# Kernel optimization log

Measured on AMD Instinct MI355X. Metric: run time of the kernel, lower is better.

## Reference

```python
import jax, jax.numpy as jnp
import numpy as np

SEQ_LEN = 2048
EMBED = 1024
HIDDEN = 1024
BATCH = 4


def setup_inputs() -> dict:
    key = jax.random.key(0)
    ks = jax.random.split(key, 7)
    # xavier_uniform for weights: limit = sqrt(6/(fan_in+fan_out))
    lim = float(np.sqrt(6.0 / (EMBED + HIDDEN)))
    blim = float(1.0 / np.sqrt(EMBED))  # torch Linear default bias init U(-1/sqrt(fan_in), ...)
    inputs = jax.random.normal(ks[0], (BATCH, SEQ_LEN, EMBED), dtype=jnp.float32)
    Wq = jax.random.uniform(ks[1], (HIDDEN, EMBED), jnp.float32, -lim, lim)
    Wk = jax.random.uniform(ks[2], (HIDDEN, EMBED), jnp.float32, -lim, lim)
    Wv = jax.random.uniform(ks[3], (HIDDEN, EMBED), jnp.float32, -lim, lim)
    bq = jax.random.uniform(ks[4], (HIDDEN,), jnp.float32, -blim, blim)
    bk = jax.random.uniform(ks[5], (HIDDEN,), jnp.float32, -blim, blim)
    bv = jax.random.uniform(ks[6], (HIDDEN,), jnp.float32, -blim, blim)
    return {"inputs": inputs, "Wq": Wq, "bq": bq, "Wk": Wk, "bk": bk, "Wv": Wv, "bv": bv}


def reference(inputs, Wq, bq, Wk, bk, Wv, bv):
    B, S, E = inputs.shape
    q = jnp.einsum('bse,he->bsh', inputs, Wq) + bq  # [B,S,H]
    k = jnp.einsum('bse,he->bsh', inputs, Wk) + bk
    v = jnp.einsum('bse,he->bsh', inputs, Wv) + bv
    # NOTE: source scales by 1/sqrt(embed_size), not hidden_size
    scores = jnp.einsum('bqh,bkh->bqk', q, k) / jnp.sqrt(jnp.float32(E))
    causal = jnp.tril(jnp.ones((S, S), dtype=bool))  # [S,S]
    scores = jnp.where(causal[None, :, :], scores, -jnp.inf)
    attn = jax.nn.softmax(scores, axis=-1)
    return jnp.einsum('bqk,bkh->bqh', attn, v)
```

## Files before the change

kernel.cpp:

```cpp
#include <hip/hip_runtime.h>
#include <cstdint>
#include <cstddef>
#include <math.h>

typedef unsigned short u16;

#define S_LEN 2048
#define EMB   1024
#define HID   1024
#define NB    4

using bf16x8 = __attribute__((ext_vector_type(8))) __bf16;
using f32x4  = __attribute__((ext_vector_type(4))) float;


__device__ __forceinline__ u16 f2bf(float f) {
  union { float f; uint32_t u; } c; c.f = f;
  uint32_t u = c.u;
  uint32_t r = (u + 0x7fffu + ((u >> 16) & 1u)) >> 16;
  return (u16)r;
}

__device__ __forceinline__ void gld_lds16(const u16* g, u16* l) {
  auto gp = (const __attribute__((address_space(1))) uint32_t*)(uintptr_t)(const void*)g;
  auto lp = (__attribute__((address_space(3))) uint32_t*)(uintptr_t)(void*)l;
  __builtin_amdgcn_global_load_lds(gp, lp, 16, 0, 0);
}


__global__ void cvt_f32_bf16(const float* __restrict__ in, u16* __restrict__ out, int n4) {
  int i = blockIdx.x * blockDim.x + threadIdx.x;
  int stride = gridDim.x * blockDim.x;
  for (; i < n4; i += stride) {
    float4 v = reinterpret_cast<const float4*>(in)[i];
    reinterpret_cast<ushort4*>(out)[i] =
      make_ushort4(f2bf(v.x), f2bf(v.y), f2bf(v.z), f2bf(v.w));
  }
}

__global__ void cvt3_f32_bf16(const float* __restrict__ a, const float* __restrict__ b,
                              const float* __restrict__ c, u16* __restrict__ out, int n4) {
  const float* src = (blockIdx.y == 0) ? a : (blockIdx.y == 1) ? b : c;
  u16* dst = out + (size_t)blockIdx.y * (size_t)n4 * 4;
  int i = blockIdx.x * blockDim.x + threadIdx.x;
  int stride = gridDim.x * blockDim.x;
  for (; i < n4; i += stride) {
    float4 v = reinterpret_cast<const float4*>(src)[i];
    reinterpret_cast<ushort4*>(dst)[i] =
      make_ushort4(f2bf(v.x), f2bf(v.y), f2bf(v.z), f2bf(v.w));
  }
}


template<int EPI>
__global__ __launch_bounds__(512, 2)
void gemmT(const u16* __restrict__ A, const u16* __restrict__ Bw, void* __restrict__ Cv,
           const float* __restrict__ b0, const float* __restrict__ b1,
           const float* __restrict__ b2, u16* __restrict__ VT,
           int N, long sA, long sB, long sC, float scale)
{
  constexpr int K = 1024;
  constexpr int NTILE = K / 64;
  const int z = blockIdx.z;
  A  += (long)z * sA;
  Bw += (long)z * sB;

  __shared__ __align__(16) u16 smem[32768];

  const int tid = threadIdx.x;
  const int l   = tid & 63;
  const int w   = tid >> 6;
  const int wr  = w >> 2;
  const int wc  = w & 3;

  int bm, bn;
  if constexpr (EPI == 2) {
    const int x0 = blockIdx.x;
    const int x  = (x0 & 7) * ((int)gridDim.x >> 3) + (x0 >> 3);
    int bi = (int)((sqrtf(8.0f * (float)x + 1.0f) - 1.0f) * 0.5f);
    while ((bi + 1) * (bi + 2) / 2 <= x) ++bi;
    while (bi * (bi + 1) / 2 > x) --bi;
    bm = bi * 128;
    bn = (x - bi * (bi + 1) / 2) * 128;
  } else {
    const int nwg = gridDim.x * gridDim.y;
    const int lin = blockIdx.y * gridDim.x + blockIdx.x;
    const int sw  = (lin & 7) * (nwg >> 3) + (lin >> 3);
    bm = (sw / gridDim.x) * 128;
    bn = (sw % gridDim.x) * 128;
  }

  const int arow = w * 16 + (l >> 2);
  const int acs  = (l & 3) ^ (((l >> 5) & 1) << 1);
  const u16* gbA = A  + (long)(bm + arow) * K + acs * 8;
  const u16* gbB = Bw + (long)(bn + arow) * K + acs * 8;

#define STGH(t, s, dbase)                                                       \
  do {                                                                          \
    const long _o = (long)(t) * 64 + (s) * 32;                                  \
    gld_lds16(gbA + _o, smem + (dbase) + (s) * 4096 + w * 512);                 \
    gld_lds16(gbB + _o, smem + (dbase) + 8192 + (s) * 4096 + w * 512);          \
  } while (0)

  const int lr  = l & 15;
  const int kg  = l >> 4;
  const int kgp = kg ^ (((lr >> 3) & 1) << 1);
  int aoff[4], boff[2];
#pragma unroll
  for (int m = 0; m < 4; ++m) aoff[m] = (wr * 64 + m * 16 + lr) * 32 + kgp * 8;
#pragma unroll
  for (int n = 0; n < 2; ++n) boff[n] = (wc * 32 + n * 16 + lr) * 32 + kgp * 8;

  f32x4 acc[4][2] = {};

  STGH(0, 0, 0);
  STGH(0, 1, 0);
  asm volatile("s_waitcnt vmcnt(0)" ::: "memory");
  __builtin_amdgcn_s_barrier();
  asm volatile("" ::: "memory");

#define PHASE(d, s, STGSTMT)                                                    \
  do {                                                                          \
    const u16* hA = smem + (d) * 16384 + (s) * 4096;                            \
    const u16* hB = smem + (d) * 16384 + 8192 + (s) * 4096;                     \
    bf16x8 av[4], bv[2];                                                        \
    _Pragma("unroll")                                                           \
    for (int m_ = 0; m_ < 4; ++m_)                                              \
      av[m_] = *reinterpret_cast<const bf16x8*>(hA + aoff[m_]);                 \
    _Pragma("unroll")                                                           \
    for (int n_ = 0; n_ < 2; ++n_)                                              \
      bv[n_] = *reinterpret_cast<const bf16x8*>(hB + boff[n_]);                 \
    STGSTMT;                                                                    \
    asm volatile("s_waitcnt vmcnt(2)" ::: "memory");                            \
    __builtin_amdgcn_s_barrier();                                               \
    asm volatile("" ::: "memory");                                              \
    __builtin_amdgcn_s_setprio(1);                                              \
    _Pragma("unroll")                                                           \
    for (int m_ = 0; m_ < 4; ++m_)                                              \
      _Pragma("unroll")                                                         \
      for (int n_ = 0; n_ < 2; ++n_)                                            \
        acc[m_][n_] = __builtin_amdgcn_mfma_f32_16x16x32_bf16(                  \
            av[m_], bv[n_], acc[m_][n_], 0, 0, 0);                              \
    __builtin_amdgcn_s_setprio(0);                                              \
    asm volatile("" ::: "memory");                                              \
  } while (0)

#pragma unroll 1
  for (int i = 0; i < NTILE / 2; ++i) {
    const int t1 = 2 * i + 1;
    const int t2 = (2 * i + 2 < NTILE) ? 2 * i + 2 : NTILE - 1;
    PHASE(0, 0, STGH(t1, 0, 16384));
    PHASE(0, 1, STGH(t1, 1, 16384));
    PHASE(1, 0, STGH(t2, 0, 0));
    PHASE(1, 1, STGH(t2, 1, 0));
  }
#undef PHASE
#undef STGH

  if constexpr (EPI == 2) {
    float* C = (float*)Cv + (long)z * sC;
#pragma unroll
    for (int n = 0; n < 2; ++n) {
      const int col = bn + wc * 32 + n * 16 + lr;
#pragma unroll
      for (int m = 0; m < 4; ++m) {
        const int row0 = bm + wr * 64 + m * 16 + kg * 4;
#pragma unroll
        for (int q = 0; q < 4; ++q) {
          const int row = row0 + q;
          float v = acc[m][n][q] * scale;
          if (col > row) v = -1e30f;
          C[(long)row * N + col] = v;
        }
      }
    }
  } else {
    constexpr long M = (long)NB * S_LEN;
    const int sel = bn >> 10;
    const float* bias = (sel == 0) ? b0 : (sel == 1) ? b1 : b2;
    u16* QK = (u16*)Cv;
#pragma unroll
    for (int n = 0; n < 2; ++n) {
      const int col = bn + wc * 32 + n * 16 + lr;
      const int h   = col & (HID - 1);
      const float bbv = bias[h];
#pragma unroll
      for (int m = 0; m < 4; ++m) {
        const int row0 = bm + wr * 64 + m * 16 + kg * 4;
        if (sel < 2) {
          u16* dst = QK + (long)sel * M * HID + (long)row0 * HID + h;
#pragma unroll
          for (int q = 0; q < 4; ++q)
            dst[(long)q * HID] = f2bf(acc[m][n][q] + bbv);
        } else {
          const int b = row0 >> 11;
          const int s = row0 & (S_LEN - 1);
          ushort4 o = make_ushort4(f2bf(acc[m][n][0] + bbv), f2bf(acc[m][n][1] + bbv),
                                   f2bf(acc[m][n][2] + bbv), f2bf(acc[m][n][3] + bbv));
          *reinterpret_cast<ushort4*>(VT + ((long)b * HID + h) * S_LEN + s) = o;
        }
      }
    }
  }
}


__global__ __launch_bounds__(512, 2)
void gemm_pv(const u16* __restrict__ Pm, const u16* __restrict__ VTm, float* __restrict__ Cm)
{
  const int z = blockIdx.z;
  const u16* A = Pm  + (long)z * S_LEN * S_LEN;
  const u16* B = VTm + (long)z * HID * S_LEN;
  float*    Cz = Cm  + (long)z * S_LEN * HID;

  __shared__ __align__(16) u16 smem[32768];

  const int tid = threadIdx.x;
  const int l   = tid & 63;
  const int w   = tid >> 6;
  const int wr  = w >> 2;
  const int wc  = w & 3;
  const int bn  = blockIdx.x * 128;
  const int pr  = blockIdx.y;

  const int lr  = l & 15;
  const int kg  = l >> 4;
  const int kgp = kg ^ (((lr >> 3) & 1) << 1);
  int aoff[4], boff[2];
#pragma unroll
  for (int m = 0; m < 4; ++m) aoff[m] = (wr * 64 + m * 16 + lr) * 32 + kgp * 8;
#pragma unroll
  for (int n = 0; n < 2; ++n) boff[n] = (wc * 32 + n * 16 + lr) * 32 + kgp * 8;

  const int arow = w * 16 + (l >> 2);
  const int acs  = (l & 3) ^ (((l >> 5) & 1) << 1);

#pragma unroll 1
  for (int it = 0; it < 2; ++it) {
    const int bi = (it == 0) ? (15 - pr) : pr;
    const int bm = bi * 128;
    const int NTILE = (bi + 1) * 2;

    const u16* gbA = A + (long)(bm + arow) * S_LEN + acs * 8;
    const u16* gbB = B + (long)(bn + arow) * S_LEN + acs * 8;

#define STGH(t, s, dbase)                                                       \
  do {                                                                          \
    const long _o = (long)(t) * 64 + (s) * 32;                                  \
    gld_lds16(gbA + _o, smem + (dbase) + (s) * 4096 + w * 512);                 \
    gld_lds16(gbB + _o, smem + (dbase) + 8192 + (s) * 4096 + w * 512);          \
  } while (0)

    if (it) {
      __builtin_amdgcn_s_barrier();
      asm volatile("" ::: "memory");
    }

    f32x4 acc[4][2] = {};

    STGH(0, 0, 0);
    STGH(0, 1, 0);
    asm volatile("s_waitcnt vmcnt(0)" ::: "memory");
    __builtin_amdgcn_s_barrier();
    asm volatile("" ::: "memory");

#define PHASE(d, s, STGSTMT)                                                    \
  do {                                                                          \
    const u16* hA = smem + (d) * 16384 + (s) * 4096;                            \
    const u16* hB = smem + (d) * 16384 + 8192 + (s) * 4096;                     \
    bf16x8 av[4], bv[2];                                                        \
    _Pragma("unroll")                                                           \
    for (int m_ = 0; m_ < 4; ++m_)                                              \
      av[m_] = *reinterpret_cast<const bf16x8*>(hA + aoff[m_]);                 \
    _Pragma("unroll")                                                           \
    for (int n_ = 0; n_ < 2; ++n_)                                              \
      bv[n_] = *reinterpret_cast<const bf16x8*>(hB + boff[n_]);                 \
    STGSTMT;                                                                    \
    asm volatile("s_waitcnt vmcnt(2)" ::: "memory");                            \
    __builtin_amdgcn_s_barrier();                                               \
    asm volatile("" ::: "memory");                                              \
    __builtin_amdgcn_s_setprio(1);                                              \
    _Pragma("unroll")                                                           \
    for (int m_ = 0; m_ < 4; ++m_)                                              \
      _Pragma("unroll")                                                         \
      for (int n_ = 0; n_ < 2; ++n_)                                            \
        acc[m_][n_] = __builtin_amdgcn_mfma_f32_16x16x32_bf16(                  \
            av[m_], bv[n_], acc[m_][n_], 0, 0, 0);                              \
    __builtin_amdgcn_s_setprio(0);                                              \
    asm volatile("" ::: "memory");                                              \
  } while (0)

#pragma unroll 1
    for (int i = 0; i < NTILE / 2; ++i) {
      const int t1 = 2 * i + 1;
      const int t2 = (2 * i + 2 < NTILE) ? 2 * i + 2 : NTILE - 1;
      PHASE(0, 0, STGH(t1, 0, 16384));
      PHASE(0, 1, STGH(t1, 1, 16384));
      PHASE(1, 0, STGH(t2, 0, 0));
      PHASE(1, 1, STGH(t2, 1, 0));
    }
#undef PHASE
#undef STGH

#pragma unroll
    for (int n = 0; n < 2; ++n) {
      const int col = bn + wc * 32 + n * 16 + lr;
#pragma unroll
      for (int m = 0; m < 4; ++m) {
        const int row0 = bm + wr * 64 + m * 16 + kg * 4;
#pragma unroll
        for (int q = 0; q < 4; ++q)
          Cz[(long)(row0 + q) * HID + col] = acc[m][n][q];
      }
    }
  }
}


__global__ __launch_bounds__(256)
void softmax_causal(const float* __restrict__ Sc, u16* __restrict__ P, long sS, long sP)
{
  const int row  = blockIdx.x;
  const int z    = blockIdx.y;
  const int kend = ((row >> 7) + 1) << 7;
  const float* srow = Sc + (long)z * sS + (long)row * S_LEN;
  u16*        prow = P  + (long)z * sP + (long)row * S_LEN;
  const int t = threadIdx.x;
  const int lane = t & 63, wave = t >> 6;

  const bool p0 = (4 * t) < kend;
  const bool p1 = (1024 + 4 * t) < kend;

  float4 v0 = make_float4(-1e30f, -1e30f, -1e30f, -1e30f);
  float4 v1 = v0;
  if (p0) v0 = reinterpret_cast<const float4*>(srow)[t];
  if (p1) v1 = reinterpret_cast<const float4*>(srow)[t + 256];

  float mx = fmaxf(fmaxf(fmaxf(v0.x, v0.y), fmaxf(v0.z, v0.w)),
                   fmaxf(fmaxf(v1.x, v1.y), fmaxf(v1.z, v1.w)));

  __shared__ float red[8];
#pragma unroll
  for (int off = 32; off; off >>= 1) mx = fmaxf(mx, __shfl_down(mx, off));
  if (lane == 0) red[wave] = mx;
  __syncthreads();
  mx = fmaxf(fmaxf(red[0], red[1]), fmaxf(red[2], red[3]));

  float e[8];
  e[0] = __expf(v0.x - mx); e[1] = __expf(v0.y - mx);
  e[2] = __expf(v0.z - mx); e[3] = __expf(v0.w - mx);
  e[4] = __expf(v1.x - mx); e[5] = __expf(v1.y - mx);
  e[6] = __expf(v1.z - mx); e[7] = __expf(v1.w - mx);

  float sm = ((e[0] + e[1]) + (e[2] + e[3])) + ((e[4] + e[5]) + (e[6] + e[7]));
#pragma unroll
  for (int off = 32; off; off >>= 1) sm += __shfl_down(sm, off);
  if (lane == 0) red[4 + wave] = sm;
  __syncthreads();
  sm = (red[4] + red[5]) + (red[6] + red[7]);

  const float inv = 1.0f / sm;
  if (p0)
    reinterpret_cast<ushort4*>(prow)[t] =
      make_ushort4(f2bf(e[0]*inv), f2bf(e[1]*inv), f2bf(e[2]*inv), f2bf(e[3]*inv));
  if (p1)
    reinterpret_cast<ushort4*>(prow)[t + 256] =
      make_ushort4(f2bf(e[4]*inv), f2bf(e[5]*inv), f2bf(e[6]*inv), f2bf(e[7]*inv));
}


extern "C" void kernel_launch(void* const* d_in, const int* in_sizes, int n_in,
                              void* d_out, int out_size, void* d_ws, size_t ws_size,
                              hipStream_t stream)
{
  const float* x  = (const float*)d_in[0];
  const float* Wq = (const float*)d_in[1];
  const float* bq = (const float*)d_in[2];
  const float* Wk = (const float*)d_in[3];
  const float* bk = (const float*)d_in[4];
  const float* Wv = (const float*)d_in[5];
  const float* bv = (const float*)d_in[6];
  float* out = (float*)d_out;

  const long M = (long)NB * S_LEN;

  u16* xb  = (u16*)d_ws;
  u16* wqb = xb  + M * EMB;
  u16* Qb  = wqb + 3L * HID * EMB;
  u16* Kb  = Qb  + M * HID;
  u16* VT  = Kb  + M * HID;
  char* rest = (char*)(VT + M * HID);
  const size_t used  = (size_t)(rest - (char*)d_ws);
  const size_t ssz   = (size_t)S_LEN * S_LEN;
  const size_t need4 = used + (size_t)NB * ssz * 4 + (size_t)NB * ssz * 2;
  const int nb = (ws_size >= need4) ? NB : 1;
  float* scores = (float*)rest;
  u16*   P      = (u16*)(rest + (size_t)nb * ssz * 4);

  cvt_f32_bf16<<<2048, 256, 0, stream>>>(x, xb, (int)(M * EMB / 4));
  cvt3_f32_bf16<<<dim3(512, 3), 256, 0, stream>>>(Wq, Wk, Wv, wqb, HID * EMB / 4);

  gemmT<4><<<dim3(24, 64, 1), 512, 0, stream>>>(xb, wqb, Qb, bq, bk, bv, VT,
                                                3 * HID, 0, 0, 0, 1.0f);

  const float scale = 0.03125f;
  const int TRI = 16 * 17 / 2;

  if (nb == NB) {
    dim3 gs(TRI, 1, NB);
    gemmT<2><<<gs, 512, 0, stream>>>(Qb, Kb, scores, nullptr, nullptr, nullptr, nullptr,
                                     S_LEN, (long)S_LEN * HID, (long)S_LEN * HID,
                                     (long)ssz, scale);
    softmax_causal<<<dim3(S_LEN, NB), 256, 0, stream>>>(scores, P, (long)ssz, (long)ssz);
    gemm_pv<<<dim3(8, 8, NB), 512, 0, stream>>>(P, VT, out);
  } else {
    for (int b = 0; b < NB; ++b) {
      const u16* Qbb = Qb + (long)b * S_LEN * HID;
      const u16* Kbb = Kb + (long)b * S_LEN * HID;
      const u16* VTb = VT + (long)b * HID * S_LEN;
      float* outb = out + (long)b * S_LEN * HID;
      dim3 gs(TRI, 1, 1);
      gemmT<2><<<gs, 512, 0, stream>>>(Qbb, Kbb, scores, nullptr, nullptr, nullptr, nullptr,
                                       S_LEN, 0, 0, 0, scale);
      softmax_causal<<<dim3(S_LEN, 1), 256, 0, stream>>>(scores, P, 0, 0);
      gemm_pv<<<dim3(8, 8, 1), 512, 0, stream>>>(P, VTb, outb);
    }
  }
}
```

Baseline: 159.7 us.

## Use 4-wave 64x64 warp tiles in gemmT and merge conversion kernels

The gemmT kernel now runs 256 threads (4 waves) per 128x128 block instead of 8. Each wave computes a 64x64 sub-tile (4x4 MFMA fragments) and issues twice as many global-to-LDS loads, which raises LDS fragment reuse per wave but uses more accumulator registers. The x and weight fp32-to-bf16 conversions are also merged into a single launch to drop one kernel dispatch. The risks are lower latency hiding from fewer waves and higher register pressure under launch_bounds(256,2).

```diff
diff --git a/kernel.cpp b/kernel.cpp
--- a/kernel.cpp
+++ b/kernel.cpp
@@ -28,32 +28,32 @@
 }
 
 
-__global__ void cvt_f32_bf16(const float* __restrict__ in, u16* __restrict__ out, int n4) {
+__global__ void cvt_all(const float* __restrict__ x,  const float* __restrict__ wq,
+                        const float* __restrict__ wk, const float* __restrict__ wv,
+                        u16* __restrict__ xb, u16* __restrict__ wb, int nx4, int nw4lg2) {
+  const int nw4 = 1 << nw4lg2;
+  const int total = nx4 + 3 * nw4;
   int i = blockIdx.x * blockDim.x + threadIdx.x;
-  int stride = gridDim.x * blockDim.x;
-  for (; i < n4; i += stride) {
-    float4 v = reinterpret_cast<const float4*>(in)[i];
-    reinterpret_cast<ushort4*>(out)[i] =
+  const int stride = gridDim.x * blockDim.x;
+  for (; i < total; i += stride) {
+    const float* src; u16* dst; int j;
+    if (i < nx4) { src = x; dst = xb; j = i; }
+    else {
+      const int k = i - nx4;
+      const int wsel = k >> nw4lg2;
+      j = k & (nw4 - 1);
+      src = (wsel == 0) ? wq : (wsel == 1) ? wk : wv;
+      dst = wb + ((size_t)wsel << (nw4lg2 + 2));
+    }
+    float4 v = reinterpret_cast<const float4*>(src)[j];
+    reinterpret_cast<ushort4*>(dst)[j] =
       make_ushort4(f2bf(v.x), f2bf(v.y), f2bf(v.z), f2bf(v.w));
   }
 }
 
-__global__ void cvt3_f32_bf16(const float* __restrict__ a, const float* __restrict__ b,
-                              const float* __restrict__ c, u16* __restrict__ out, int n4) {
-  const float* src = (blockIdx.y == 0) ? a : (blockIdx.y == 1) ? b : c;
-  u16* dst = out + (size_t)blockIdx.y * (size_t)n4 * 4;
-  int i = blockIdx.x * blockDim.x + threadIdx.x;
-  int stride = gridDim.x * blockDim.x;
-  for (; i < n4; i += stride) {
-    float4 v = reinterpret_cast<const float4*>(src)[i];
-    reinterpret_cast<ushort4*>(dst)[i] =
-      make_ushort4(f2bf(v.x), f2bf(v.y), f2bf(v.z), f2bf(v.w));
-  }
-}
-
 
 template<int EPI>
-__global__ __launch_bounds__(512, 2)
+__global__ __launch_bounds__(256, 2)
 void gemmT(const u16* __restrict__ A, const u16* __restrict__ Bw, void* __restrict__ Cv,
            const float* __restrict__ b0, const float* __restrict__ b1,
            const float* __restrict__ b2, u16* __restrict__ VT,
@@ -70,8 +70,8 @@
   const int tid = threadIdx.x;
   const int l   = tid & 63;
   const int w   = tid >> 6;
-  const int wr  = w >> 2;
-  const int wc  = w & 3;
+  const int wr  = w >> 1;
+  const int wc  = w & 1;
 
   int bm, bn;
   if constexpr (EPI == 2) {
@@ -92,26 +92,30 @@
 
   const int arow = w * 16 + (l >> 2);
   const int acs  = (l & 3) ^ (((l >> 5) & 1) << 1);
-  const u16* gbA = A  + (long)(bm + arow) * K + acs * 8;
-  const u16* gbB = Bw + (long)(bn + arow) * K + acs * 8;
+  const u16* gbA  = A  + (long)(bm + arow) * K + acs * 8;
+  const u16* gbA2 = gbA + 64L * K;
+  const u16* gbB  = Bw + (long)(bn + arow) * K + acs * 8;
+  const u16* gbB2 = gbB + 64L * K;
 
 #define STGH(t, s, dbase)                                                       \
   do {                                                                          \
     const long _o = (long)(t) * 64 + (s) * 32;                                  \
-    gld_lds16(gbA + _o, smem + (dbase) + (s) * 4096 + w * 512);                 \
-    gld_lds16(gbB + _o, smem + (dbase) + 8192 + (s) * 4096 + w * 512);          \
+    gld_lds16(gbA  + _o, smem + (dbase) + (s) * 4096 +        w * 512);         \
+    gld_lds16(gbA2 + _o, smem + (dbase) + (s) * 4096 + 2048 + w * 512);         \
+    gld_lds16(gbB  + _o, smem + (dbase) + 8192 + (s) * 4096 +        w * 512);  \
+    gld_lds16(gbB2 + _o, smem + (dbase) + 8192 + (s) * 4096 + 2048 + w * 512);  \
   } while (0)
 
   const int lr  = l & 15;
   const int kg  = l >> 4;
   const int kgp = kg ^ (((lr >> 3) & 1) << 1);
-  int aoff[4], boff[2];
+  int aoff[4], boff[4];
 #pragma unroll
   for (int m = 0; m < 4; ++m) aoff[m] = (wr * 64 + m * 16 + lr) * 32 + kgp * 8;
 #pragma unroll
-  for (int n = 0; n < 2; ++n) boff[n] = (wc * 32 + n * 16 + lr) * 32 + kgp * 8;
-
-  f32x4 acc[4][2] = {};
+  for (int n = 0; n < 4; ++n) boff[n] = (wc * 64 + n * 16 + lr) * 32 + kgp * 8;
+
+  f32x4 acc[4][4] = {};
 
   STGH(0, 0, 0);
   STGH(0, 1, 0);
@@ -123,22 +127,22 @@
   do {                                                                          \
     const u16* hA = smem + (d) * 16384 + (s) * 4096;                            \
     const u16* hB = smem + (d) * 16384 + 8192 + (s) * 4096;                     \
-    bf16x8 av[4], bv[2];                                                        \
+    bf16x8 av[4], bv[4];                                                        \
     _Pragma("unroll")                                                           \
     for (int m_ = 0; m_ < 4; ++m_)                                              \
       av[m_] = *reinterpret_cast<const bf16x8*>(hA + aoff[m_]);                 \
     _Pragma("unroll")                                                           \
-    for (int n_ = 0; n_ < 2; ++n_)                                              \
+    for (int n_ = 0; n_ < 4; ++n_)                                              \
       bv[n_] = *reinterpret_cast<const bf16x8*>(hB + boff[n_]);                 \
     STGSTMT;                                                                    \
-    asm volatile("s_waitcnt vmcnt(2)" ::: "memory");                            \
+    asm volatile("s_waitcnt vmcnt(4)" ::: "memory");                            \
     __builtin_amdgcn_s_barrier();                                               \
     asm volatile("" ::: "memory");                                              \
     __builtin_amdgcn_s_setprio(1);                                              \
     _Pragma("unroll")                                                           \
     for (int m_ = 0; m_ < 4; ++m_)                                              \
       _Pragma("unroll")                                                         \
-      for (int n_ = 0; n_ < 2; ++n_)                                            \
+      for (int n_ = 0; n_ < 4; ++n_)                                            \
         acc[m_][n_] = __builtin_amdgcn_mfma_f32_16x16x32_bf16(                  \
             av[m_], bv[n_], acc[m_][n_], 0, 0, 0);                              \
     __builtin_amdgcn_s_setprio(0);                                              \
@@ -160,8 +164,8 @@
   if constexpr (EPI == 2) {
     float* C = (float*)Cv + (long)z * sC;
 #pragma unroll
-    for (int n = 0; n < 2; ++n) {
-      const int col = bn + wc * 32 + n * 16 + lr;
+    for (int n = 0; n < 4; ++n) {
+      const int col = bn + wc * 64 + n * 16 + lr;
 #pragma unroll
       for (int m = 0; m < 4; ++m) {
         const int row0 = bm + wr * 64 + m * 16 + kg * 4;
@@ -180,8 +184,8 @@
     const float* bias = (sel == 0) ? b0 : (sel == 1) ? b1 : b2;
     u16* QK = (u16*)Cv;
 #pragma unroll
-    for (int n = 0; n < 2; ++n) {
-      const int col = bn + wc * 32 + n * 16 + lr;
+    for (int n = 0; n < 4; ++n) {
+      const int col = bn + wc * 64 + n * 16 + lr;
       const int h   = col & (HID - 1);
       const float bbv = bias[h];
 #pragma unroll
@@ -397,10 +401,9 @@
   float* scores = (float*)rest;
   u16*   P      = (u16*)(rest + (size_t)nb * ssz * 4);
 
-  cvt_f32_bf16<<<2048, 256, 0, stream>>>(x, xb, (int)(M * EMB / 4));
-  cvt3_f32_bf16<<<dim3(512, 3), 256, 0, stream>>>(Wq, Wk, Wv, wqb, HID * EMB / 4);
-
-  gemmT<4><<<dim3(24, 64, 1), 512, 0, stream>>>(xb, wqb, Qb, bq, bk, bv, VT,
+  cvt_all<<<2048, 256, 0, stream>>>(x, Wq, Wk, Wv, xb, wqb, (int)(M * EMB / 4), 18);
+
+  gemmT<4><<<dim3(24, 64, 1), 256, 0, stream>>>(xb, wqb, Qb, bq, bk, bv, VT,
                                                 3 * HID, 0, 0, 0, 1.0f);
 
   const float scale = 0.03125f;
@@ -408,7 +411,7 @@
 
   if (nb == NB) {
     dim3 gs(TRI, 1, NB);
-    gemmT<2><<<gs, 512, 0, stream>>>(Qb, Kb, scores, nullptr, nullptr, nullptr, nullptr,
+    gemmT<2><<<gs, 256, 0, stream>>>(Qb, Kb, scores, nullptr, nullptr, nullptr, nullptr,
                                      S_LEN, (long)S_LEN * HID, (long)S_LEN * HID,
                                      (long)ssz, scale);
     softmax_causal<<<dim3(S_LEN, NB), 256, 0, stream>>>(scores, P, (long)ssz, (long)ssz);
@@ -420,7 +423,7 @@
       const u16* VTb = VT + (long)b * HID * S_LEN;
       float* outb = out + (long)b * S_LEN * HID;
       dim3 gs(TRI, 1, 1);
-      gemmT<2><<<gs, 512, 0, stream>>>(Qbb, Kbb, scores, nullptr, nullptr, nullptr, nullptr,
+      gemmT<2><<<gs, 256, 0, stream>>>(Qbb, Kbb, scores, nullptr, nullptr, nullptr, nullptr,
                                        S_LEN, 0, 0, 0, scale);
       softmax_causal<<<dim3(S_LEN, 1), 256, 0, stream>>>(scores, P, 0, 0);
       gemm_pv<<<dim3(8, 8, 1), 512, 0, stream>>>(P, VTb, outb);
```

Measured after the change: 160.2 us. About the same (+0.3%).
